# Optimization experiments

Measured on AMD Instinct MI355X. Metric: run time of the kernel, lower is better.

Reference implementation:

```python
import jax, jax.numpy as jnp
import numpy as np

P, G, UV = 5, 40000, 256          # n_parts, gs_num (visible UV texels), uv_size
ZD, FD, HD = 32, 64, 32           # latent_z_dim, latent_f_dim, latent_h_dim
H1, L1 = 128, 3                   # mlp1 hidden dim, fc layers
H2, L2 = 128, 3                   # mlp2 hidden dim, fc layers
CC, LC = 64, 4                    # cnn hidden channels, cnn hidden layers


def _mlp_params(key, din, hid, nlayers, dout, nparts):
    ks = jax.random.split(key, 3)
    s = lambda f: 1.0 / np.sqrt(f)
    return dict(
        w_in=jax.random.normal(ks[0], (nparts, din, hid), jnp.float32) * s(din),
        b_in=jnp.zeros((nparts, hid), jnp.float32),
        w_hid=jax.random.normal(ks[1], (nparts, nlayers - 1, hid, hid), jnp.float32) * s(hid),
        b_hid=jnp.zeros((nparts, nlayers - 1, hid), jnp.float32),
        w_out=jax.random.normal(ks[2], (nparts, hid, dout), jnp.float32) * s(hid),
        b_out=jnp.zeros((nparts, dout), jnp.float32),
    )


def setup_inputs() -> dict:
    key = jax.random.key(0)
    ks = jax.random.split(key, 12)
    d1 = FD + ZD
    d2 = d1 + 3 + 11
    inp = {
        'latent_z': jax.random.normal(ks[2], (G, ZD), jnp.float32),
        'latent_f': jax.random.normal(ks[3], (P, FD), jnp.float32),
        'cano_xyz': jax.random.normal(ks[4], (G, 3), jnp.float32),
    }
    for k, v in _mlp_params(ks[0], d1, H1, L1, 11, P).items():
        inp['mlp1_' + k] = v
    for k, v in _mlp_params(ks[1], d2, H2, L2, HD, P).items():
        inp['mlp2_' + k] = v
    inp['conv_in_w'] = jax.random.normal(ks[5], (CC, HD, 3, 3), jnp.float32) * (1.0 / np.sqrt(HD * 9))
    inp['conv_in_b'] = jnp.zeros((CC,), jnp.float32)
    inp['conv_hid_w'] = jax.random.normal(ks[6], (LC - 1, CC, CC, 3, 3), jnp.float32) * (1.0 / np.sqrt(CC * 9))
    inp['conv_hid_b'] = jnp.zeros((LC - 1, CC), jnp.float32)
    inp['conv_out_w'] = jax.random.normal(ks[7], (3, CC, 3, 3), jnp.float32) * (1.0 / np.sqrt(CC * 9))
    inp['conv_out_b'] = jnp.zeros((3,), jnp.float32)
    inp['gs_part'] = jax.random.randint(ks[8], (G,), 0, P, jnp.int32)
    inp['uv_idx'] = jax.random.permutation(ks[9], UV * UV)[:G].astype(jnp.int32)  # unique visible texels
    return inp


def _part_mlp(x, w_in, b_in, w_hid, b_hid, w_out, b_out, part):
    # x: [G, D]; weights stacked over parts. Run every part's MLP, gather by part id.
    h = jax.nn.leaky_relu(jnp.einsum('gd,pdh->pgh', x, w_in) + b_in[:, None, :])
    for l in range(w_hid.shape[1]):
        h = jax.nn.leaky_relu(jnp.einsum('pgh,pho->pgo', h, w_hid[:, l]) + b_hid[:, l][:, None, :])
    out = jnp.einsum('pgh,pho->pgo', h, w_out) + b_out[:, None, :]  # [P, G, O]
    return out[part, jnp.arange(out.shape[1])]                       # [G, O]


def _conv(x, w, b):
    y = jax.lax.conv_general_dilated(x, w, (1, 1), 'SAME',
                                     dimension_numbers=('NCHW', 'OIHW', 'NCHW'))
    return y + b[None, :, None, None]


def _instance_norm(x, eps=1e-5):
    m = x.mean(axis=(2, 3), keepdims=True)
    v = x.var(axis=(2, 3), keepdims=True)
    return (x - m) / jnp.sqrt(v + eps)


def reference(latent_z, latent_f, cano_xyz,
              mlp1_w_in, mlp1_b_in, mlp1_w_hid, mlp1_b_hid, mlp1_w_out, mlp1_b_out,
              mlp2_w_in, mlp2_b_in, mlp2_w_hid, mlp2_b_hid, mlp2_w_out, mlp2_b_out,
              conv_in_w, conv_in_b, conv_hid_w, conv_hid_b, conv_out_w, conv_out_b,
              gs_part, uv_idx):
    feat_f = latent_f[gs_part]                                  # [G, FD] per-part feature gather
    x1 = jnp.concatenate([feat_f, latent_z], axis=-1)           # [G, FD+ZD]
    attrs = _part_mlp(x1, mlp1_w_in, mlp1_b_in, mlp1_w_hid, mlp1_b_hid,
                      mlp1_w_out, mlp1_b_out, gs_part)          # [G, 11] gaussian attrs
    x2 = jnp.concatenate([x1, cano_xyz, attrs], axis=-1)        # [G, FD+ZD+3+11]
    h = _part_mlp(x2, mlp2_w_in, mlp2_b_in, mlp2_w_hid, mlp2_b_hid,
                  mlp2_w_out, mlp2_b_out, gs_part)              # [G, HD]
    # scatter per-gaussian features back into the UV map (uvmask-indexed texels)
    uvmap = jnp.zeros((UV * UV, h.shape[-1]), h.dtype).at[uv_idx].add(h)
    x = uvmap.T.reshape(1, h.shape[-1], UV, UV)                 # [1, HD, UV, UV]
    # CNN refinement: conv -> (relu, conv, instance_norm) x (LC-1) -> conv -> sigmoid
    x = _conv(x, conv_in_w, conv_in_b)
    for l in range(conv_hid_w.shape[0]):
        x = _instance_norm(_conv(jax.nn.relu(x), conv_hid_w[l], conv_hid_b[l]))
    x = _conv(x, conv_out_w, conv_out_b)
    return jax.nn.sigmoid(x)                                    # [1, 3, UV, UV]
```

## Files before the change

kernel.cpp:

```cpp
#include <hip/hip_runtime.h>

#define G_N 40000
#define P_N 5
#define PIX 65536
#define XP 136

typedef short short8 __attribute__((ext_vector_type(8)));
typedef short short4v __attribute__((ext_vector_type(4)));
typedef float f32x4 __attribute__((ext_vector_type(4)));
#define MFMA16(a, b, c) __builtin_amdgcn_mfma_f32_16x16x32_bf16(a, b, c, 0, 0, 0)

__device__ __forceinline__ short f2b(float f) {
    unsigned u = __builtin_bit_cast(unsigned, f);
    unsigned r = (u + 0x7fffu + ((u >> 16) & 1u)) >> 16;
    return (short)r;
}
__device__ __forceinline__ float b2f(short s) {
    unsigned u = ((unsigned)(unsigned short)s) << 16;
    return __builtin_bit_cast(float, u);
}


__global__ __launch_bounds__(256) void hist_k(const int* __restrict__ part,
                                              int* __restrict__ counts, int n) {
    __shared__ int s_c[P_N];
    if (threadIdx.x < P_N) s_c[threadIdx.x] = 0;
    __syncthreads();
    int g = blockIdx.x * 256 + threadIdx.x;
    if (g < n) atomicAdd(&s_c[part[g]], 1);
    __syncthreads();
    if (threadIdx.x < P_N) atomicAdd(&counts[threadIdx.x], s_c[threadIdx.x]);
}

__global__ void offs_k(const int* __restrict__ counts, int* __restrict__ offs) {
    if (threadIdx.x == 0) {
        int o = 0;
        for (int p = 0; p < P_N; ++p) {
            offs[p] = o;
            o += (counts[p] + 127) & ~127;
        }
        offs[P_N] = o;
    }
}

__global__ __launch_bounds__(256) void scatter_k(const int* __restrict__ part,
                                                 const int* __restrict__ offs,
                                                 int* __restrict__ cursors,
                                                 int* __restrict__ perm, int n) {
    const int t = threadIdx.x;
    const int g = blockIdx.x * 256 + t;
    const int p = (g < n) ? part[g] : -1;
    const int lane = t & 63;
    const int wid = t >> 6;
    __shared__ int s_wc[4][P_N];
    __shared__ int s_base[P_N];
    const unsigned long long lmask = (1ull << lane) - 1ull;
    int myrank = 0;
    for (int pp = 0; pp < P_N; ++pp) {
        unsigned long long m = __ballot(p == pp);
        if (p == pp) myrank = __popcll(m & lmask);
        if (lane == 0) s_wc[wid][pp] = __popcll(m);
    }
    __syncthreads();
    if (t < P_N) {
        int tot = s_wc[0][t] + s_wc[1][t] + s_wc[2][t] + s_wc[3][t];
        s_base[t] = atomicAdd(&cursors[t], tot);
    }
    __syncthreads();
    if (g < n) {
        int pre = 0;
        #pragma unroll
        for (int w2 = 0; w2 < 4; ++w2) if (w2 < wid) pre += s_wc[w2][p];
        perm[offs[p] + s_base[p] + pre + myrank] = g;
    }
}


__device__ __forceinline__ float mseg(int l, const float* __restrict__ src,
                                      int DIN, int DOUT, int NP, int pps) {
    const int pn = NP * 128;
    const int p = l / pn;
    const int r = l - p * pn;
    const int n = r >> 7, k = r & 127;
    return (n < DOUT && k < DIN) ? src[p * pps + k * DOUT + n] : 0.f;
}
__device__ __forceinline__ float cseg(int l, const float* __restrict__ src, int CIN) {
    const int per = 9 * 64 * CIN;
    const int ll = l / per;
    int rem = l - ll * per;
    const int tap = rem / (64 * CIN);
    rem -= tap * 64 * CIN;
    const int och = rem / CIN;
    const int ci = rem - och * CIN;
    return src[((ll * 64 + och) * CIN + ci) * 9 + tap];
}

__global__ __launch_bounds__(256) void prep_k(
        const float* __restrict__ m1wi, const float* __restrict__ m1wh,
        const float* __restrict__ m1wo, const float* __restrict__ m2wi,
        const float* __restrict__ m2wh, const float* __restrict__ m2wo,
        const float* __restrict__ cinw, const float* __restrict__ chw,
        short* __restrict__ wb) {
    const int idx = blockIdx.x * 256 + threadIdx.x;
    if (idx >= 651264) return;
    float v;
    if      (idx < 81920)  v = mseg(idx,          m1wi,         96, 128, 128, 12288);
    else if (idx < 163840) v = mseg(idx - 81920,  m1wh,        128, 128, 128, 32768);
    else if (idx < 245760) v = mseg(idx - 163840, m1wh + 16384,128, 128, 128, 32768);
    else if (idx < 256000) v = mseg(idx - 245760, m1wo,        128,  11,  16, 1408);
    else if (idx < 337920) v = mseg(idx - 256000, m2wi,        110, 128, 128, 14080);
    else if (idx < 419840) v = mseg(idx - 337920, m2wh,        128, 128, 128, 32768);
    else if (idx < 501760) v = mseg(idx - 419840, m2wh + 16384,128, 128, 128, 32768);
    else if (idx < 522240) v = mseg(idx - 501760, m2wo,        128,  32,  32, 4096);
    else if (idx < 540672) v = cseg(idx - 522240, cinw, 32);
    else                   v = cseg(idx - 540672, chw, 64);
    wb[idx] = f2b(v);
}


template<int NKC, bool ACT>
__device__ __forceinline__ void dlayerSep(const short* __restrict__ wt,
                                          const float* __restrict__ bias,
                                          const short* src, short* dst, int m0, int n0) {
    const int lane = threadIdx.x & 63;
    const int ln = lane & 15, lq = lane >> 4;
    short8 B[4][NKC];
    float bs[4];
    #pragma unroll
    for (int nt = 0; nt < 4; ++nt) {
        #pragma unroll
        for (int kc = 0; kc < NKC; ++kc)
            B[nt][kc] = *(const short8*)(wt + (n0 + nt * 16 + ln) * 128 + kc * 32 + lq * 8);
        bs[nt] = bias[n0 + nt * 16 + ln];
    }
    #pragma unroll
    for (int mt = 0; mt < 4; ++mt) {
        short8 A[NKC];
        #pragma unroll
        for (int kc = 0; kc < NKC; ++kc)
            A[kc] = *(const short8*)(src + (m0 + mt * 16 + ln) * XP + kc * 32 + lq * 8);
        #pragma unroll
        for (int nt = 0; nt < 4; ++nt) {
            f32x4 acc = {bs[nt], bs[nt], bs[nt], bs[nt]};
            #pragma unroll
            for (int kc = 0; kc < NKC; ++kc)
                acc = MFMA16(A[kc], B[nt][kc], acc);
            #pragma unroll
            for (int r = 0; r < 4; ++r) {
                float v = acc[r];
                if (ACT) v = fmaxf(v, 0.01f * v);
                dst[(m0 + mt * 16 + lq * 4 + r) * XP + n0 + nt * 16 + ln] = f2b(v);
            }
        }
    }
}

template<bool ACT>
__device__ __forceinline__ void dlayerIP(const short* __restrict__ wt,
                                         const float* __restrict__ bias,
                                         short* buf, int m0, int n0) {
    const int lane = threadIdx.x & 63;
    const int ln = lane & 15, lq = lane >> 4;
    short8 A[4][4];
    #pragma unroll
    for (int mt = 0; mt < 4; ++mt)
        #pragma unroll
        for (int kc = 0; kc < 4; ++kc)
            A[mt][kc] = *(const short8*)(buf + (m0 + mt * 16 + ln) * XP + kc * 32 + lq * 8);
    __syncthreads();
    #pragma unroll
    for (int nt = 0; nt < 4; ++nt) {
        short8 B[4];
        #pragma unroll
        for (int kc = 0; kc < 4; ++kc)
            B[kc] = *(const short8*)(wt + (n0 + nt * 16 + ln) * 128 + kc * 32 + lq * 8);
        const float bs = bias[n0 + nt * 16 + ln];
        #pragma unroll
        for (int mt = 0; mt < 4; ++mt) {
            f32x4 acc = {bs, bs, bs, bs};
            #pragma unroll
            for (int kc = 0; kc < 4; ++kc)
                acc = MFMA16(A[mt][kc], B[kc], acc);
            #pragma unroll
            for (int r = 0; r < 4; ++r) {
                float v = acc[r];
                if (ACT) v = fmaxf(v, 0.01f * v);
                buf[(m0 + mt * 16 + lq * 4 + r) * XP + n0 + nt * 16 + ln] = f2b(v);
            }
        }
    }
    __syncthreads();
}

__global__ __launch_bounds__(256) void mlp_k(
        const float* __restrict__ latent_z, const float* __restrict__ latent_f,
        const float* __restrict__ cano,
        const short* __restrict__ wt1i, const float* __restrict__ b1i,
        const short* __restrict__ wt1h0, const short* __restrict__ wt1h1,
        const float* __restrict__ b1h,
        const short* __restrict__ wt1o, const float* __restrict__ b1o,
        const short* __restrict__ wt2i, const float* __restrict__ b2i,
        const short* __restrict__ wt2h0, const short* __restrict__ wt2h1,
        const float* __restrict__ b2h,
        const short* __restrict__ wt2o, const float* __restrict__ b2o,
        const int* __restrict__ uv_idx, const int* __restrict__ perm,
        const int* __restrict__ offs, const int* __restrict__ counts,
        unsigned short* __restrict__ uvmap ) {
    __shared__ short s_x[128 * XP];
    __shared__ short s_h[128 * XP];
    __shared__ int s_g[128];
    __shared__ int s_uv[128];

    const int t = threadIdx.x;
    const int lane = t & 63;
    const int w = t >> 6;
    const int ln = lane & 15, lq = lane >> 4;
    const int pos0 = blockIdx.x * 128;
    if (pos0 >= offs[P_N]) return;
    int p = 0;
    #pragma unroll
    for (int q = 1; q < P_N; ++q) if (pos0 >= offs[q]) p = q;
    const int vend = offs[p] + counts[p];

    if (t < 128) {
        const int pos = pos0 + t;
        const int g = (pos < vend) ? perm[pos] : -1;
        s_g[t] = g;
        s_uv[t] = (g >= 0) ? uv_idx[g] : 0;
    }
    __syncthreads();

    for (int i = t; i < 128 * 16; i += 256) {
        const int g = i >> 4, k4 = (i & 15) * 4;
        const float4 v = *(const float4*)(latent_f + p * 64 + k4);
        short4v o = {f2b(v.x), f2b(v.y), f2b(v.z), f2b(v.w)};
        *(short4v*)(s_x + g * XP + k4) = o;
    }
    for (int i = t; i < 128 * 8; i += 256) {
        const int g = i >> 3, k4 = (i & 7) * 4;
        const int gg = s_g[g];
        short4v o = {0, 0, 0, 0};
        if (gg >= 0) {
            const float4 v = *(const float4*)(latent_z + gg * 32 + k4);
            o[0] = f2b(v.x); o[1] = f2b(v.y); o[2] = f2b(v.z); o[3] = f2b(v.w);
        }
        *(short4v*)(s_x + g * XP + 64 + k4) = o;
    }
    for (int i = t; i < 128 * 3; i += 256) {
        const int g = i / 3, k = i - g * 3;
        const int gg = s_g[g];
        s_x[g * XP + 96 + k] = (gg >= 0) ? f2b(cano[gg * 3 + k]) : 0;
    }
    for (int i = t; i < 128 * 37; i += 256) {
        const int g = i / 37, k = 99 + (i - g * 37);
        s_x[g * XP + k] = 0;
    }
    __syncthreads();

    const int m0 = (w >> 1) * 64, n0 = (w & 1) * 64;

    dlayerSep<3, true>(wt1i + p * 16384, b1i + p * 128, s_x, s_h, m0, n0);
    __syncthreads();
    dlayerIP<true>(wt1h0 + p * 16384, b1h + (p * 2 + 0) * 128, s_h, m0, n0);
    dlayerIP<true>(wt1h1 + p * 16384, b1h + (p * 2 + 1) * 128, s_h, m0, n0);
    if ((w & 1) == 0) {
        short8 B[4];
        #pragma unroll
        for (int kc = 0; kc < 4; ++kc)
            B[kc] = *(const short8*)(wt1o + p * 2048 + ln * 128 + kc * 32 + lq * 8);
        const float bs = (ln < 11) ? b1o[p * 11 + ln] : 0.f;
        #pragma unroll
        for (int mt = 0; mt < 4; ++mt) {
            short8 A[4];
            #pragma unroll
            for (int kc = 0; kc < 4; ++kc)
                A[kc] = *(const short8*)(s_h + (m0 + mt * 16 + ln) * XP + kc * 32 + lq * 8);
            f32x4 acc = {bs, bs, bs, bs};
            #pragma unroll
            for (int kc = 0; kc < 4; ++kc) acc = MFMA16(A[kc], B[kc], acc);
            if (ln < 11) {
                #pragma unroll
                for (int r = 0; r < 4; ++r)
                    s_x[(m0 + mt * 16 + lq * 4 + r) * XP + 99 + ln] = f2b(acc[r]);
            }
        }
    }
    __syncthreads();

    dlayerSep<4, true>(wt2i + p * 16384, b2i + p * 128, s_x, s_h, m0, n0);
    __syncthreads();
    dlayerIP<true>(wt2h0 + p * 16384, b2h + (p * 2 + 0) * 128, s_h, m0, n0);
    dlayerIP<true>(wt2h1 + p * 16384, b2h + (p * 2 + 1) * 128, s_h, m0, n0);
    {
        const int nt0 = (w & 1) * 16;
        short8 B[4];
        #pragma unroll
        for (int kc = 0; kc < 4; ++kc)
            B[kc] = *(const short8*)(wt2o + p * 4096 + (nt0 + ln) * 128 + kc * 32 + lq * 8);
        const float bs = b2o[p * 32 + nt0 + ln];
        #pragma unroll
        for (int mt = 0; mt < 4; ++mt) {
            short8 A[4];
            #pragma unroll
            for (int kc = 0; kc < 4; ++kc)
                A[kc] = *(const short8*)(s_h + (m0 + mt * 16 + ln) * XP + kc * 32 + lq * 8);
            f32x4 acc = {bs, bs, bs, bs};
            #pragma unroll
            for (int kc = 0; kc < 4; ++kc) acc = MFMA16(A[kc], B[kc], acc);
            #pragma unroll
            for (int r = 0; r < 4; ++r) {
                const int m = m0 + mt * 16 + lq * 4 + r;
                const int g = s_g[m];
                if (g >= 0)
                    uvmap[s_uv[m] * 32 + nt0 + ln] = (unsigned short)f2b(acc[r]);
            }
        }
    }
}


template<int CIN, int TRANS, bool STATS>
__global__ __launch_bounds__(256, 2) void conv_k(
        const unsigned short* __restrict__ in,
        const short* __restrict__ wt,
        const float* __restrict__ bias,
        const float* __restrict__ psum, const float* __restrict__ psq,
        unsigned short* __restrict__ out,
        float* __restrict__ ssum, float* __restrict__ ssq) {
    constexpr int CS = CIN + 8;
    constexpr int NKC = CIN / 32;
    __shared__ short s_in[18 * 18 * CS];
    __shared__ float s_mr[2][64];

    const int t = threadIdx.x;
    const int lane = t & 63;
    const int ln = lane & 15, lq = lane >> 4;
    const int tx0 = blockIdx.x * 16, ty0 = blockIdx.y * 16;
    const int och0 = blockIdx.z * 32;

    short8 B[9][NKC][2];
    #pragma unroll
    for (int tap = 0; tap < 9; ++tap)
        #pragma unroll
        for (int kc = 0; kc < NKC; ++kc)
            #pragma unroll
            for (int nt = 0; nt < 2; ++nt)
                B[tap][kc][nt] = *(const short8*)(wt +
                    (tap * 64 + och0 + nt * 16 + ln) * CIN + kc * 32 + lq * 8);

    if (TRANS == 2 && t < 64) {
        const float m = psum[t] * (1.f / PIX);
        const float vv = psq[t] * (1.f / PIX) - m * m;
        s_mr[0][t] = m;
        s_mr[1][t] = rsqrtf(vv + 1e-5f);
    }
    if (TRANS == 2) __syncthreads();

    constexpr int RUNS = CIN / 8;
    for (int i = t; i < 324 * RUNS; i += 256) {
        const int sp = i / RUNS, run = i - sp * RUNS;
        const int r = sp / 18, c = sp - r * 18;
        const int gy = ty0 + r - 1, gx = tx0 + c - 1;
        short* dst = &s_in[(r * 18 + c) * CS + run * 8];
        if (gy >= 0 && gy < 256 && gx >= 0 && gx < 256) {
            short8 v = *(const short8*)(in + ((gy * 256 + gx) * CIN + run * 8));
            if (TRANS == 0) {
                *(short8*)dst = v;
            } else {
                short8 o;
                #pragma unroll
                for (int j = 0; j < 8; ++j) {
                    float f = b2f(v[j]);
                    if (TRANS == 2) f = (f - s_mr[0][run * 8 + j]) * s_mr[1][run * 8 + j];
                    o[j] = f2b(fmaxf(f, 0.f));
                }
                *(short8*)dst = o;
            }
        } else {
            short8 z = {0, 0, 0, 0, 0, 0, 0, 0};
            *(short8*)dst = z;
        }
    }
    __syncthreads();

    f32x4 acc[4][2];
    {
        float bs[2];
        #pragma unroll
        for (int nt = 0; nt < 2; ++nt) bs[nt] = bias[och0 + nt * 16 + ln];
        #pragma unroll
        for (int mt = 0; mt < 4; ++mt)
            #pragma unroll
            for (int nt = 0; nt < 2; ++nt) {
                f32x4 a = {bs[nt], bs[nt], bs[nt], bs[nt]};
                acc[mt][nt] = a;
            }
    }

    const int r0 = (t >> 6) * 4;
    #pragma unroll
    for (int tap = 0; tap < 9; ++tap) {
        const int dy = tap / 3, dx = tap - dy * 3;
        #pragma unroll
        for (int kc = 0; kc < NKC; ++kc) {
            short8 A[4];
            #pragma unroll
            for (int mt = 0; mt < 4; ++mt)
                A[mt] = *(const short8*)&s_in[((r0 + mt + dy) * 18 + ln + dx) * CS + kc * 32 + lq * 8];
            #pragma unroll
            for (int mt = 0; mt < 4; ++mt)
                #pragma unroll
                for (int nt = 0; nt < 2; ++nt)
                    acc[mt][nt] = MFMA16(A[mt], B[tap][kc][nt], acc[mt][nt]);
        }
    }

    #pragma unroll
    for (int nt = 0; nt < 2; ++nt) {
        float lsum = 0.f, lsqs = 0.f;
        #pragma unroll
        for (int mt = 0; mt < 4; ++mt) {
            const int gy = ty0 + r0 + mt;
            #pragma unroll
            for (int r = 0; r < 4; ++r) {
                const float v = acc[mt][nt][r];
                const int gx = tx0 + lq * 4 + r;
                out[(gy * 256 + gx) * 64 + och0 + nt * 16 + ln] = (unsigned short)f2b(v);
                if (STATS) { lsum += v; lsqs = fmaf(v, v, lsqs); }
            }
        }
        if (STATS) {
            lsum += __shfl_xor(lsum, 16, 64);
            lsum += __shfl_xor(lsum, 32, 64);
            lsqs += __shfl_xor(lsqs, 16, 64);
            lsqs += __shfl_xor(lsqs, 32, 64);
            if (lq == 0) {
                atomicAdd(&ssum[och0 + nt * 16 + ln], lsum);
                atomicAdd(&ssq[och0 + nt * 16 + ln], lsqs);
            }
        }
    }
}

__global__ __launch_bounds__(256) void convout_k(
        const unsigned short* __restrict__ in,
        const float* __restrict__ w,
        const float* __restrict__ bias,
        const float* __restrict__ psum, const float* __restrict__ psq,
        float* __restrict__ out) {
    constexpr int CS = 72;
    __shared__ short s_in[18 * 18 * CS];
    __shared__ float s_w[3][9][64];
    __shared__ float s_mr[2][64];

    const int t = threadIdx.x;
    const int tx0 = blockIdx.x * 16, ty0 = blockIdx.y * 16;
    if (t < 64) {
        const float m = psum[t] * (1.f / PIX);
        const float vv = psq[t] * (1.f / PIX) - m * m;
        s_mr[0][t] = m;
        s_mr[1][t] = rsqrtf(vv + 1e-5f);
    }
    __syncthreads();

    for (int i = t; i < 324 * 8; i += 256) {
        const int sp = i >> 3, run = i & 7;
        const int r = sp / 18, c = sp - r * 18;
        const int gy = ty0 + r - 1, gx = tx0 + c - 1;
        short* dst = &s_in[(r * 18 + c) * CS + run * 8];
        if (gy >= 0 && gy < 256 && gx >= 0 && gx < 256) {
            short8 v = *(const short8*)(in + ((gy * 256 + gx) * 64 + run * 8));
            short8 o;
            #pragma unroll
            for (int j = 0; j < 8; ++j) {
                const float f = (b2f(v[j]) - s_mr[0][run * 8 + j]) * s_mr[1][run * 8 + j];
                o[j] = f2b(f);
            }
            *(short8*)dst = o;
        } else {
            short8 z = {0, 0, 0, 0, 0, 0, 0, 0};
            *(short8*)dst = z;
        }
    }
    for (int i = t; i < 1728; i += 256) {
        const int o = i / 576;
        const int rem = i - o * 576;
        const int tap = rem >> 6;
        const int ci = rem & 63;
        s_w[o][tap][ci] = w[o * 576 + ci * 9 + tap];
    }
    __syncthreads();

    const int py = t >> 4, px = t & 15;
    float a0 = bias[0], a1 = bias[1], a2 = bias[2];
    for (int tap = 0; tap < 9; ++tap) {
        const int dy = tap / 3, dx = tap % 3;
        const short* rp = &s_in[((py + dy) * 18 + (px + dx)) * CS];
        #pragma unroll
        for (int c8 = 0; c8 < 8; ++c8) {
            short8 v = *(const short8*)(rp + c8 * 8);
            #pragma unroll
            for (int j = 0; j < 8; ++j) {
                const float f = b2f(v[j]);
                const int ci = c8 * 8 + j;
                a0 = fmaf(f, s_w[0][tap][ci], a0);
                a1 = fmaf(f, s_w[1][tap][ci], a1);
                a2 = fmaf(f, s_w[2][tap][ci], a2);
            }
        }
    }
    const int pix = (ty0 + py) * 256 + tx0 + px;
    out[pix]           = 1.f / (1.f + expf(-a0));
    out[PIX + pix]     = 1.f / (1.f + expf(-a1));
    out[2 * PIX + pix] = 1.f / (1.f + expf(-a2));
}


extern "C" void kernel_launch(void* const* d_in, const int* in_sizes, int n_in,
                              void* d_out, int out_size, void* d_ws, size_t ws_size,
                              hipStream_t stream) {
    (void)in_sizes; (void)n_in; (void)out_size; (void)ws_size;
    const float* latent_z = (const float*)d_in[0];
    const float* latent_f = (const float*)d_in[1];
    const float* cano     = (const float*)d_in[2];
    const float* m1wi = (const float*)d_in[3];
    const float* m1bi = (const float*)d_in[4];
    const float* m1wh = (const float*)d_in[5];
    const float* m1bh = (const float*)d_in[6];
    const float* m1wo = (const float*)d_in[7];
    const float* m1bo = (const float*)d_in[8];
    const float* m2wi = (const float*)d_in[9];
    const float* m2bi = (const float*)d_in[10];
    const float* m2wh = (const float*)d_in[11];
    const float* m2bh = (const float*)d_in[12];
    const float* m2wo = (const float*)d_in[13];
    const float* m2bo = (const float*)d_in[14];
    const float* cinw = (const float*)d_in[15];
    const float* cinb = (const float*)d_in[16];
    const float* chw  = (const float*)d_in[17];
    const float* chb  = (const float*)d_in[18];
    const float* cow  = (const float*)d_in[19];
    const float* cob  = (const float*)d_in[20];
    const int* gs_part = (const int*)d_in[21];
    const int* uv_idx  = (const int*)d_in[22];

    float* ws = (float*)d_ws;
    unsigned short* actA = (unsigned short*)ws;
    unsigned short* actB = (unsigned short*)(ws + 2097152);
    unsigned short* uvmap = actB;

    short* wb = (short*)(ws + 4194304);
    short* wt1i  = wb;
    short* wt1h0 = wb + 81920;
    short* wt1h1 = wb + 163840;
    short* wt1o  = wb + 245760;
    short* wt2i  = wb + 256000;
    short* wt2h0 = wb + 337920;
    short* wt2h1 = wb + 419840;
    short* wt2o  = wb + 501760;
    short* cwt_in  = wb + 522240;
    short* cwt_hid = wb + 540672;

    float* small = ws + 4194304 + 330000;
    int* counts  = (int*)small;
    int* cursors = counts + 8;
    int* offs    = cursors + 8;
    float* ssum  = small + 32;
    float* ssq   = ssum + 192;
    int* perm    = (int*)(ssq + 192);

    hipMemsetAsync(uvmap, 0, (size_t)PIX * 32 * sizeof(unsigned short), stream);
    hipMemsetAsync(small, 0, 1024 * sizeof(float), stream);

    hist_k<<<157, 256, 0, stream>>>(gs_part, counts, G_N);
    offs_k<<<1, 64, 0, stream>>>(counts, offs);
    scatter_k<<<157, 256, 0, stream>>>(gs_part, offs, cursors, perm, G_N);

    prep_k<<<2544, 256, 0, stream>>>(m1wi, m1wh, m1wo, m2wi, m2wh, m2wo, cinw, chw, wb);

    mlp_k<<<318, 256, 0, stream>>>(latent_z, latent_f, cano,
        wt1i, m1bi, wt1h0, wt1h1, m1bh, wt1o, m1bo,
        wt2i, m2bi, wt2h0, wt2h1, m2bh, wt2o, m2bo,
        uv_idx, perm, offs, counts, uvmap);

    dim3 cgrid(16, 16, 2);
    conv_k<32, 0, false><<<cgrid, 256, 0, stream>>>(uvmap, cwt_in, cinb,
        nullptr, nullptr, actA, nullptr, nullptr);
    conv_k<64, 1, true><<<cgrid, 256, 0, stream>>>(actA, cwt_hid, chb,
        nullptr, nullptr, actB, ssum, ssq);
    conv_k<64, 2, true><<<cgrid, 256, 0, stream>>>(actB, cwt_hid + 36864, chb + 64,
        ssum, ssq, actA, ssum + 64, ssq + 64);
    conv_k<64, 2, true><<<cgrid, 256, 0, stream>>>(actA, cwt_hid + 73728, chb + 128,
        ssum + 64, ssq + 64, actB, ssum + 128, ssq + 128);
    convout_k<<<dim3(16, 16), 256, 0, stream>>>(actB, cow, cob,
        ssum + 128, ssq + 128, (float*)d_out);
}
```

Measured before the change: 292.2 us.

## Shrink MLP tiles to single-wave blocks and retile convs to 16x8 full-channel

```diff
diff --git a/kernel.cpp b/kernel.cpp
--- a/kernel.cpp
+++ b/kernel.cpp
@@ -4,6 +4,7 @@
 #define P_N 5
 #define PIX 65536
 #define XP 136
+#define SP 40
 
 typedef short short8 __attribute__((ext_vector_type(8)));
 typedef short short4v __attribute__((ext_vector_type(4)));
@@ -37,7 +38,7 @@
         int o = 0;
         for (int p = 0; p < P_N; ++p) {
             offs[p] = o;
-            o += (counts[p] + 127) & ~127;
+            o += (counts[p] + 63) & ~63;
         }
         offs[P_N] = o;
     }
@@ -119,80 +120,43 @@
 
 
 template<int NKC, bool ACT>
-__device__ __forceinline__ void dlayerSep(const short* __restrict__ wt,
-                                          const float* __restrict__ bias,
-                                          const short* src, short* dst, int m0, int n0) {
-    const int lane = threadIdx.x & 63;
-    const int ln = lane & 15, lq = lane >> 4;
-    short8 B[4][NKC];
-    float bs[4];
+__device__ __forceinline__ void wcompute(const short8 (&A)[4][NKC],
+                                         const short* __restrict__ wt,
+                                         const float* __restrict__ bias,
+                                         short* dst) {
+    const int ln = threadIdx.x & 15, lq = threadIdx.x >> 4;
     #pragma unroll
-    for (int nt = 0; nt < 4; ++nt) {
+    for (int nt = 0; nt < 8; ++nt) {
+        short8 B[NKC];
         #pragma unroll
         for (int kc = 0; kc < NKC; ++kc)
-            B[nt][kc] = *(const short8*)(wt + (n0 + nt * 16 + ln) * 128 + kc * 32 + lq * 8);
-        bs[nt] = bias[n0 + nt * 16 + ln];
-    }
-    #pragma unroll
-    for (int mt = 0; mt < 4; ++mt) {
-        short8 A[NKC];
-        #pragma unroll
-        for (int kc = 0; kc < NKC; ++kc)
-            A[kc] = *(const short8*)(src + (m0 + mt * 16 + ln) * XP + kc * 32 + lq * 8);
-        #pragma unroll
-        for (int nt = 0; nt < 4; ++nt) {
-            f32x4 acc = {bs[nt], bs[nt], bs[nt], bs[nt]};
-            #pragma unroll
-            for (int kc = 0; kc < NKC; ++kc)
-                acc = MFMA16(A[kc], B[nt][kc], acc);
+            B[kc] = *(const short8*)(wt + (nt * 16 + ln) * 128 + kc * 32 + lq * 8);
+        const float bs = bias[nt * 16 + ln];
+        #pragma unroll
+        for (int mt = 0; mt < 4; ++mt) {
+            f32x4 acc = {bs, bs, bs, bs};
+            #pragma unroll
+            for (int kc = 0; kc < NKC; ++kc) acc = MFMA16(A[mt][kc], B[kc], acc);
             #pragma unroll
             for (int r = 0; r < 4; ++r) {
                 float v = acc[r];
                 if (ACT) v = fmaxf(v, 0.01f * v);
-                dst[(m0 + mt * 16 + lq * 4 + r) * XP + n0 + nt * 16 + ln] = f2b(v);
-            }
-        }
-    }
-}
-
-template<bool ACT>
-__device__ __forceinline__ void dlayerIP(const short* __restrict__ wt,
-                                         const float* __restrict__ bias,
-                                         short* buf, int m0, int n0) {
-    const int lane = threadIdx.x & 63;
-    const int ln = lane & 15, lq = lane >> 4;
-    short8 A[4][4];
+                dst[(mt * 16 + lq * 4 + r) * XP + nt * 16 + ln] = f2b(v);
+            }
+        }
+    }
+}
+
+__device__ __forceinline__ void preload4(short8 (&A)[4][4], const short* s) {
+    const int ln = threadIdx.x & 15, lq = threadIdx.x >> 4;
     #pragma unroll
     for (int mt = 0; mt < 4; ++mt)
         #pragma unroll
         for (int kc = 0; kc < 4; ++kc)
-            A[mt][kc] = *(const short8*)(buf + (m0 + mt * 16 + ln) * XP + kc * 32 + lq * 8);
-    __syncthreads();
-    #pragma unroll
-    for (int nt = 0; nt < 4; ++nt) {
-        short8 B[4];
-        #pragma unroll
-        for (int kc = 0; kc < 4; ++kc)
-            B[kc] = *(const short8*)(wt + (n0 + nt * 16 + ln) * 128 + kc * 32 + lq * 8);
-        const float bs = bias[n0 + nt * 16 + ln];
-        #pragma unroll
-        for (int mt = 0; mt < 4; ++mt) {
-            f32x4 acc = {bs, bs, bs, bs};
-            #pragma unroll
-            for (int kc = 0; kc < 4; ++kc)
-                acc = MFMA16(A[mt][kc], B[kc], acc);
-            #pragma unroll
-            for (int r = 0; r < 4; ++r) {
-                float v = acc[r];
-                if (ACT) v = fmaxf(v, 0.01f * v);
-                buf[(m0 + mt * 16 + lq * 4 + r) * XP + n0 + nt * 16 + ln] = f2b(v);
-            }
-        }
-    }
-    __syncthreads();
-}
-
-__global__ __launch_bounds__(256) void mlp_k(
+            A[mt][kc] = *(const short8*)(s + (mt * 16 + ln) * XP + kc * 32 + lq * 8);
+}
+
+__global__ __launch_bounds__(64, 2) void mlp_k(
         const float* __restrict__ latent_z, const float* __restrict__ latent_f,
         const float* __restrict__ cano,
         const short* __restrict__ wt1i, const float* __restrict__ b1i,
@@ -206,37 +170,36 @@
         const int* __restrict__ uv_idx, const int* __restrict__ perm,
         const int* __restrict__ offs, const int* __restrict__ counts,
         unsigned short* __restrict__ uvmap ) {
-    __shared__ short s_x[128 * XP];
-    __shared__ short s_h[128 * XP];
-    __shared__ int s_g[128];
-    __shared__ int s_uv[128];
+    __shared__ short s_h[64 * XP];
+    __shared__ short s_c4[64 * SP];
+    __shared__ int s_g[64];
+    __shared__ int s_uv[64];
 
     const int t = threadIdx.x;
-    const int lane = t & 63;
-    const int w = t >> 6;
-    const int ln = lane & 15, lq = lane >> 4;
-    const int pos0 = blockIdx.x * 128;
+    const int ln = t & 15, lq = t >> 4;
+    const int pos0 = blockIdx.x * 64;
     if (pos0 >= offs[P_N]) return;
     int p = 0;
     #pragma unroll
     for (int q = 1; q < P_N; ++q) if (pos0 >= offs[q]) p = q;
     const int vend = offs[p] + counts[p];
 
-    if (t < 128) {
+    {
         const int pos = pos0 + t;
         const int g = (pos < vend) ? perm[pos] : -1;
         s_g[t] = g;
         s_uv[t] = (g >= 0) ? uv_idx[g] : 0;
     }
-    __syncthreads();
-
-    for (int i = t; i < 128 * 16; i += 256) {
+    for (int i = t; i < 64 * SP / 2; i += 64) ((int*)s_c4)[i] = 0;
+    __syncthreads();
+
+    for (int i = t; i < 64 * 16; i += 64) {
         const int g = i >> 4, k4 = (i & 15) * 4;
         const float4 v = *(const float4*)(latent_f + p * 64 + k4);
         short4v o = {f2b(v.x), f2b(v.y), f2b(v.z), f2b(v.w)};
-        *(short4v*)(s_x + g * XP + k4) = o;
-    }
-    for (int i = t; i < 128 * 8; i += 256) {
+        *(short4v*)(s_h + g * XP + k4) = o;
+    }
+    for (int i = t; i < 64 * 8; i += 64) {
         const int g = i >> 3, k4 = (i & 7) * 4;
         const int gg = s_g[g];
         short4v o = {0, 0, 0, 0};
@@ -244,26 +207,34 @@
             const float4 v = *(const float4*)(latent_z + gg * 32 + k4);
             o[0] = f2b(v.x); o[1] = f2b(v.y); o[2] = f2b(v.z); o[3] = f2b(v.w);
         }
-        *(short4v*)(s_x + g * XP + 64 + k4) = o;
-    }
-    for (int i = t; i < 128 * 3; i += 256) {
+        *(short4v*)(s_h + g * XP + 64 + k4) = o;
+    }
+    for (int i = t; i < 64 * 3; i += 64) {
         const int g = i / 3, k = i - g * 3;
         const int gg = s_g[g];
-        s_x[g * XP + 96 + k] = (gg >= 0) ? f2b(cano[gg * 3 + k]) : 0;
-    }
-    for (int i = t; i < 128 * 37; i += 256) {
-        const int g = i / 37, k = 99 + (i - g * 37);
-        s_x[g * XP + k] = 0;
-    }
-    __syncthreads();
-
-    const int m0 = (w >> 1) * 64, n0 = (w & 1) * 64;
-
-    dlayerSep<3, true>(wt1i + p * 16384, b1i + p * 128, s_x, s_h, m0, n0);
-    __syncthreads();
-    dlayerIP<true>(wt1h0 + p * 16384, b1h + (p * 2 + 0) * 128, s_h, m0, n0);
-    dlayerIP<true>(wt1h1 + p * 16384, b1h + (p * 2 + 1) * 128, s_h, m0, n0);
-    if ((w & 1) == 0) {
+        s_c4[g * SP + k] = (gg >= 0) ? f2b(cano[gg * 3 + k]) : 0;
+    }
+    __syncthreads();
+
+    short8 A1[4][3];
+    #pragma unroll
+    for (int mt = 0; mt < 4; ++mt)
+        #pragma unroll
+        for (int kc = 0; kc < 3; ++kc)
+            A1[mt][kc] = *(const short8*)(s_h + (mt * 16 + ln) * XP + kc * 32 + lq * 8);
+    __syncthreads();
+
+    wcompute<3, true>(A1, wt1i + p * 16384, b1i + p * 128, s_h);
+    __syncthreads();
+    {
+        short8 Ah[4][4];
+        preload4(Ah, s_h); __syncthreads();
+        wcompute<4, true>(Ah, wt1h0 + p * 16384, b1h + (p * 2 + 0) * 128, s_h);
+        __syncthreads();
+        preload4(Ah, s_h); __syncthreads();
+        wcompute<4, true>(Ah, wt1h1 + p * 16384, b1h + (p * 2 + 1) * 128, s_h);
+        __syncthreads();
+        preload4(Ah, s_h); __syncthreads();
         short8 B[4];
         #pragma unroll
         for (int kc = 0; kc < 4; ++kc)
@@ -271,48 +242,57 @@
         const float bs = (ln < 11) ? b1o[p * 11 + ln] : 0.f;
         #pragma unroll
         for (int mt = 0; mt < 4; ++mt) {
-            short8 A[4];
-            #pragma unroll
-            for (int kc = 0; kc < 4; ++kc)
-                A[kc] = *(const short8*)(s_h + (m0 + mt * 16 + ln) * XP + kc * 32 + lq * 8);
             f32x4 acc = {bs, bs, bs, bs};
             #pragma unroll
-            for (int kc = 0; kc < 4; ++kc) acc = MFMA16(A[kc], B[kc], acc);
+            for (int kc = 0; kc < 4; ++kc) acc = MFMA16(Ah[mt][kc], B[kc], acc);
             if (ln < 11) {
                 #pragma unroll
                 for (int r = 0; r < 4; ++r)
-                    s_x[(m0 + mt * 16 + lq * 4 + r) * XP + 99 + ln] = f2b(acc[r]);
-            }
-        }
-    }
-    __syncthreads();
-
-    dlayerSep<4, true>(wt2i + p * 16384, b2i + p * 128, s_x, s_h, m0, n0);
-    __syncthreads();
-    dlayerIP<true>(wt2h0 + p * 16384, b2h + (p * 2 + 0) * 128, s_h, m0, n0);
-    dlayerIP<true>(wt2h1 + p * 16384, b2h + (p * 2 + 1) * 128, s_h, m0, n0);
+                    s_c4[(mt * 16 + lq * 4 + r) * SP + 3 + ln] = f2b(acc[r]);
+            }
+        }
+    }
+    __syncthreads();
+
     {
-        const int nt0 = (w & 1) * 16;
-        short8 B[4];
-        #pragma unroll
-        for (int kc = 0; kc < 4; ++kc)
-            B[kc] = *(const short8*)(wt2o + p * 4096 + (nt0 + ln) * 128 + kc * 32 + lq * 8);
-        const float bs = b2o[p * 32 + nt0 + ln];
+        short8 A2[4][4];
         #pragma unroll
         for (int mt = 0; mt < 4; ++mt) {
-            short8 A[4];
+            A2[mt][0] = A1[mt][0]; A2[mt][1] = A1[mt][1]; A2[mt][2] = A1[mt][2];
+            A2[mt][3] = *(const short8*)(s_c4 + (mt * 16 + ln) * SP + lq * 8);
+        }
+        __syncthreads();
+        wcompute<4, true>(A2, wt2i + p * 16384, b2i + p * 128, s_h);
+    }
+    __syncthreads();
+    {
+        short8 Ah[4][4];
+        preload4(Ah, s_h); __syncthreads();
+        wcompute<4, true>(Ah, wt2h0 + p * 16384, b2h + (p * 2 + 0) * 128, s_h);
+        __syncthreads();
+        preload4(Ah, s_h); __syncthreads();
+        wcompute<4, true>(Ah, wt2h1 + p * 16384, b2h + (p * 2 + 1) * 128, s_h);
+        __syncthreads();
+        preload4(Ah, s_h);
+        #pragma unroll
+        for (int nt = 0; nt < 2; ++nt) {
+            short8 B[4];
             #pragma unroll
             for (int kc = 0; kc < 4; ++kc)
-                A[kc] = *(const short8*)(s_h + (m0 + mt * 16 + ln) * XP + kc * 32 + lq * 8);
-            f32x4 acc = {bs, bs, bs, bs};
-            #pragma unroll
-            for (int kc = 0; kc < 4; ++kc) acc = MFMA16(A[kc], B[kc], acc);
-            #pragma unroll
-            for (int r = 0; r < 4; ++r) {
-                const int m = m0 + mt * 16 + lq * 4 + r;
-                const int g = s_g[m];
-                if (g >= 0)
-                    uvmap[s_uv[m] * 32 + nt0 + ln] = (unsigned short)f2b(acc[r]);
+                B[kc] = *(const short8*)(wt2o + p * 4096 + (nt * 16 + ln) * 128 + kc * 32 + lq * 8);
+            const float bs = b2o[p * 32 + nt * 16 + ln];
+            #pragma unroll
+            for (int mt = 0; mt < 4; ++mt) {
+                f32x4 acc = {bs, bs, bs, bs};
+                #pragma unroll
+                for (int kc = 0; kc < 4; ++kc) acc = MFMA16(Ah[mt][kc], B[kc], acc);
+                #pragma unroll
+                for (int r = 0; r < 4; ++r) {
+                    const int m = mt * 16 + lq * 4 + r;
+                    const int g = s_g[m];
+                    if (g >= 0)
+                        uvmap[s_uv[m] * 32 + nt * 16 + ln] = (unsigned short)f2b(acc[r]);
+                }
             }
         }
     }
@@ -320,7 +300,7 @@
 
 
 template<int CIN, int TRANS, bool STATS>
-__global__ __launch_bounds__(256, 2) void conv_k(
+__global__ __launch_bounds__(128, 2) void conv_k(
         const unsigned short* __restrict__ in,
         const short* __restrict__ wt,
         const float* __restrict__ bias,
@@ -329,24 +309,15 @@
         float* __restrict__ ssum, float* __restrict__ ssq) {
     constexpr int CS = CIN + 8;
     constexpr int NKC = CIN / 32;
-    __shared__ short s_in[18 * 18 * CS];
+    constexpr int RUNS = CIN / 8;
+    __shared__ short s_in[10 * 18 * CS];
     __shared__ float s_mr[2][64];
+    __shared__ float s_red[2][2][64];
 
     const int t = threadIdx.x;
-    const int lane = t & 63;
-    const int ln = lane & 15, lq = lane >> 4;
-    const int tx0 = blockIdx.x * 16, ty0 = blockIdx.y * 16;
-    const int och0 = blockIdx.z * 32;
-
-    short8 B[9][NKC][2];
-    #pragma unroll
-    for (int tap = 0; tap < 9; ++tap)
-        #pragma unroll
-        for (int kc = 0; kc < NKC; ++kc)
-            #pragma unroll
-            for (int nt = 0; nt < 2; ++nt)
-                B[tap][kc][nt] = *(const short8*)(wt +
-                    (tap * 64 + och0 + nt * 16 + ln) * CIN + kc * 32 + lq * 8);
+    const int ln = t & 15, lq = (t >> 4) & 3;
+    const int w2 = t >> 6;
+    const int tx0 = blockIdx.x * 16, ty0 = blockIdx.y * 8;
 
     if (TRANS == 2 && t < 64) {
         const float m = psum[t] * (1.f / PIX);
@@ -356,8 +327,7 @@
     }
     if (TRANS == 2) __syncthreads();
 
-    constexpr int RUNS = CIN / 8;
-    for (int i = t; i < 324 * RUNS; i += 256) {
+    for (int i = t; i < 180 * RUNS; i += 128) {
         const int sp = i / RUNS, run = i - sp * RUNS;
         const int r = sp / 18, c = sp - r * 18;
         const int gy = ty0 + r - 1, gx = tx0 + c - 1;
@@ -383,78 +353,89 @@
     }
     __syncthreads();
 
-    f32x4 acc[4][2];
+    f32x4 acc[4][4];
     {
-        float bs[2];
-        #pragma unroll
-        for (int nt = 0; nt < 2; ++nt) bs[nt] = bias[och0 + nt * 16 + ln];
+        float bs[4];
+        #pragma unroll
+        for (int nt = 0; nt < 4; ++nt) bs[nt] = bias[nt * 16 + ln];
         #pragma unroll
         for (int mt = 0; mt < 4; ++mt)
             #pragma unroll
-            for (int nt = 0; nt < 2; ++nt) {
+            for (int nt = 0; nt < 4; ++nt) {
                 f32x4 a = {bs[nt], bs[nt], bs[nt], bs[nt]};
                 acc[mt][nt] = a;
             }
     }
 
-    const int r0 = (t >> 6) * 4;
     #pragma unroll
     for (int tap = 0; tap < 9; ++tap) {
         const int dy = tap / 3, dx = tap - dy * 3;
+        const short* wtap = wt + tap * 64 * CIN;
         #pragma unroll
         for (int kc = 0; kc < NKC; ++kc) {
+            short8 B[4];
+            #pragma unroll
+            for (int nt = 0; nt < 4; ++nt)
+                B[nt] = *(const short8*)(wtap + (nt * 16 + ln) * CIN + kc * 32 + lq * 8);
             short8 A[4];
             #pragma unroll
             for (int mt = 0; mt < 4; ++mt)
-                A[mt] = *(const short8*)&s_in[((r0 + mt + dy) * 18 + ln + dx) * CS + kc * 32 + lq * 8];
+                A[mt] = *(const short8*)&s_in[((w2 * 4 + mt + dy) * 18 + ln + dx) * CS + kc * 32 + lq * 8];
             #pragma unroll
             for (int mt = 0; mt < 4; ++mt)
                 #pragma unroll
-                for (int nt = 0; nt < 2; ++nt)
-                    acc[mt][nt] = MFMA16(A[mt], B[tap][kc][nt], acc[mt][nt]);
+                for (int nt = 0; nt < 4; ++nt)
+                    acc[mt][nt] = MFMA16(A[mt], B[nt], acc[mt][nt]);
         }
     }
 
     #pragma unroll
-    for (int nt = 0; nt < 2; ++nt) {
-        float lsum = 0.f, lsqs = 0.f;
+    for (int nt = 0; nt < 4; ++nt) {
+        float ls = 0.f, lsq = 0.f;
         #pragma unroll
         for (int mt = 0; mt < 4; ++mt) {
-            const int gy = ty0 + r0 + mt;
+            const int gy = ty0 + w2 * 4 + mt;
             #pragma unroll
             for (int r = 0; r < 4; ++r) {
                 const float v = acc[mt][nt][r];
                 const int gx = tx0 + lq * 4 + r;
-                out[(gy * 256 + gx) * 64 + och0 + nt * 16 + ln] = (unsigned short)f2b(v);
-                if (STATS) { lsum += v; lsqs = fmaf(v, v, lsqs); }
+                out[(gy * 256 + gx) * 64 + nt * 16 + ln] = (unsigned short)f2b(v);
+                if (STATS) { ls += v; lsq = fmaf(v, v, lsq); }
             }
         }
         if (STATS) {
-            lsum += __shfl_xor(lsum, 16, 64);
-            lsum += __shfl_xor(lsum, 32, 64);
-            lsqs += __shfl_xor(lsqs, 16, 64);
-            lsqs += __shfl_xor(lsqs, 32, 64);
-            if (lq == 0) {
-                atomicAdd(&ssum[och0 + nt * 16 + ln], lsum);
-                atomicAdd(&ssq[och0 + nt * 16 + ln], lsqs);
-            }
-        }
-    }
-}
-
-__global__ __launch_bounds__(256) void convout_k(
+            ls  += __shfl_xor(ls, 16, 64);
+            ls  += __shfl_xor(ls, 32, 64);
+            lsq += __shfl_xor(lsq, 16, 64);
+            lsq += __shfl_xor(lsq, 32, 64);
+            if (lq == 0 && (t & 32) == 0) {
+                s_red[w2][0][nt * 16 + ln] = ls;
+                s_red[w2][1][nt * 16 + ln] = lsq;
+            }
+        }
+    }
+    if (STATS) {
+        __syncthreads();
+        if (t < 64) {
+            atomicAdd(&ssum[t], s_red[0][0][t] + s_red[1][0][t]);
+            atomicAdd(&ssq[t],  s_red[0][1][t] + s_red[1][1][t]);
+        }
+    }
+}
+
+__global__ __launch_bounds__(128) void convout_k(
         const unsigned short* __restrict__ in,
         const float* __restrict__ w,
         const float* __restrict__ bias,
         const float* __restrict__ psum, const float* __restrict__ psq,
         float* __restrict__ out) {
     constexpr int CS = 72;
-    __shared__ short s_in[18 * 18 * CS];
+    __shared__ short s_in[10 * 18 * CS];
     __shared__ float s_w[3][9][64];
     __shared__ float s_mr[2][64];
 
     const int t = threadIdx.x;
-    const int tx0 = blockIdx.x * 16, ty0 = blockIdx.y * 16;
+    const int tx0 = blockIdx.x * 16, ty0 = blockIdx.y * 8;
     if (t < 64) {
         const float m = psum[t] * (1.f / PIX);
         const float vv = psq[t] * (1.f / PIX) - m * m;
@@ -463,7 +444,7 @@
     }
     __syncthreads();
 
-    for (int i = t; i < 324 * 8; i += 256) {
+    for (int i = t; i < 180 * 8; i += 128) {
         const int sp = i >> 3, run = i & 7;
         const int r = sp / 18, c = sp - r * 18;
         const int gy = ty0 + r - 1, gx = tx0 + c - 1;
@@ -482,7 +463,7 @@
             *(short8*)dst = z;
         }
     }
-    for (int i = t; i < 1728; i += 256) {
+    for (int i = t; i < 1728; i += 128) {
         const int o = i / 576;
         const int rem = i - o * 576;
         const int tap = rem >> 6;
@@ -578,20 +559,20 @@
 
     prep_k<<<2544, 256, 0, stream>>>(m1wi, m1wh, m1wo, m2wi, m2wh, m2wo, cinw, chw, wb);
 
-    mlp_k<<<318, 256, 0, stream>>>(latent_z, latent_f, cano,
+    mlp_k<<<630, 64, 0, stream>>>(latent_z, latent_f, cano,
         wt1i, m1bi, wt1h0, wt1h1, m1bh, wt1o, m1bo,
         wt2i, m2bi, wt2h0, wt2h1, m2bh, wt2o, m2bo,
         uv_idx, perm, offs, counts, uvmap);
 
-    dim3 cgrid(16, 16, 2);
-    conv_k<32, 0, false><<<cgrid, 256, 0, stream>>>(uvmap, cwt_in, cinb,
+    dim3 cgrid(16, 32);
+    conv_k<32, 0, false><<<cgrid, 128, 0, stream>>>(uvmap, cwt_in, cinb,
         nullptr, nullptr, actA, nullptr, nullptr);
-    conv_k<64, 1, true><<<cgrid, 256, 0, stream>>>(actA, cwt_hid, chb,
+    conv_k<64, 1, true><<<cgrid, 128, 0, stream>>>(actA, cwt_hid, chb,
         nullptr, nullptr, actB, ssum, ssq);
-    conv_k<64, 2, true><<<cgrid, 256, 0, stream>>>(actB, cwt_hid + 36864, chb + 64,
+    conv_k<64, 2, true><<<cgrid, 128, 0, stream>>>(actB, cwt_hid + 36864, chb + 64,
         ssum, ssq, actA, ssum + 64, ssq + 64);
-    conv_k<64, 2, true><<<cgrid, 256, 0, stream>>>(actA, cwt_hid + 73728, chb + 128,
+    conv_k<64, 2, true><<<cgrid, 128, 0, stream>>>(actA, cwt_hid + 73728, chb + 128,
         ssum + 64, ssq + 64, actB, ssum + 128, ssq + 128);
-    convout_k<<<dim3(16, 16), 256, 0, stream>>>(actB, cow, cob,
+    convout_k<<<cgrid, 128, 0, stream>>>(actB, cow, cob,
         ssum + 128, ssq + 128, (float*)d_out);
 }
```

Result: faster. 262.8 us (-10.1%).
